# Optimization experiments

Measured on AMD Instinct MI355X. Metric: run time of the kernel, lower is better.

The kernel has to match this reference:

```python
import jax, jax.numpy as jnp
import numpy as np

M = 100000      # number of simplices
NNZ = 800000    # nonzeros per Laplacian (avg degree 8)
B = 2
C_IN = 64
C_OUT = 64
K1 = 3
K2 = 3


def setup_inputs() -> dict:
    key = jax.random.key(0)
    ks = jax.random.split(key, 7)
    Ll_indices = jax.random.randint(ks[0], (2, NNZ), 0, M, dtype=jnp.int32)
    Ll_values = jax.random.normal(ks[1], (NNZ,), dtype=jnp.float32) * 0.1
    Lu_indices = jax.random.randint(ks[2], (2, NNZ), 0, M, dtype=jnp.int32)
    Lu_values = jax.random.normal(ks[3], (NNZ,), dtype=jnp.float32) * 0.1
    x = jax.random.normal(ks[4], (B, C_IN, M), dtype=jnp.float32)
    theta = jax.random.normal(ks[5], (C_OUT, C_IN, K1 + K2), dtype=jnp.float32)
    bias = jnp.zeros((1, C_OUT, 1), dtype=jnp.float32)
    return {"Ll_indices": Ll_indices, "Ll_values": Ll_values,
            "Lu_indices": Lu_indices, "Lu_values": Lu_values,
            "x": x, "theta": theta, "bias": bias}


def _spmm(rows, cols, vals, x):
    # sparse (M,M) @ x along last axis; x: (B, C, M) -> (B, C, M)
    gathered = x[:, :, cols] * vals            # (B, C, nnz)
    return jnp.zeros_like(x).at[:, :, rows].add(gathered)


def _assemble_powers(K, rows, cols, vals, x):
    outs = [x]
    for _ in range(K - 1):
        outs.append(_spmm(rows, cols, vals, outs[-1]))
    return jnp.stack(outs, axis=3)             # (B, C, M, K)


def reference(Ll_indices, Ll_values, Lu_indices, Lu_values, x, theta, bias):
    X1 = _assemble_powers(K1, Ll_indices[0], Ll_indices[1], Ll_values, x)
    X2 = _assemble_powers(K2, Lu_indices[0], Lu_indices[1], Lu_values, x)
    X = jnp.concatenate((X1, X2), axis=3)      # (B, C_in, M, K1+K2)
    y = jnp.einsum('bimk,oik->bom', X, theta)  # (B, C_out, M)
    return y + bias
```

## Files before the change

kernel.cpp:

```cpp
#include <hip/hip_runtime.h>
#include <stdint.h>

#define M_SIMP 100000
#define MPAD   100064
#define NNZV   800000
#define KM5    5
#define NBH    3125
#define NBT    1563
#define NBW    40
#define NBM    6250
#define NBS    98

typedef unsigned int u32;
typedef __attribute__((ext_vector_type(8))) short short8;
typedef __attribute__((ext_vector_type(4))) float f32x4;

__device__ __forceinline__ float bf2f(u32 u){ return __uint_as_float(u << 16); }
__device__ __forceinline__ u32 f2bf(float f){
    u32 u = __float_as_uint(f);
    return (u + 0x7FFFu + ((u >> 16) & 1u)) >> 16;
}


__device__ __forceinline__ void role_hist(int h, int t, const int* __restrict__ idx,
                                          int* __restrict__ cnt, u32* __restrict__ pe){
    int e = h * 256 + t;
    if (e < NNZV){
        int r = idx[e];
        pe[e] = (u32)atomicAdd(&cnt[r], 1);
    }
}

__device__ __forceinline__ void role_transpose(int g, int t, const float* __restrict__ x,
                                               u32* __restrict__ F0){
    __shared__ unsigned short s[64 * 130];
    int m0 = g * 64;
    int j  = t & 63;
    int r4 = t >> 6;
    #pragma unroll 4
    for (int it = 0; it < 32; ++it){
        int bc = it * 4 + r4;
        int m  = m0 + j;
        if (m < M_SIMP)
            s[j * 130 + bc] = (unsigned short)f2bf(x[(size_t)bc * M_SIMP + m]);
    }
    __syncthreads();
    #pragma unroll 4
    for (int it = 0; it < 16; ++it){
        int m  = it * 4 + r4;
        int gm = m0 + m;
        if (gm < M_SIMP){
            u32 lo = s[m * 130 + 2 * j];
            u32 hi = s[m * 130 + 2 * j + 1];
            F0[(size_t)gm * 64 + j] = lo | (hi << 16);
        }
    }
}

__device__ __forceinline__ void role_wb(int g, int t, const float* __restrict__ theta,
                                        u32* __restrict__ Wb){
    int idx = g * 256 + t;
    if (idx < KM5 * 64 * 32){
        int km = idx >> 11;
        int r  = idx & 2047;
        int o  = r >> 5;
        int i2 = (r & 31) * 2;
        int k  = (km == 0) ? 0 : ((km < 3) ? km : km + 1);
        float lo = theta[o * 384 + i2 * 6 + k];
        float hi = theta[o * 384 + (i2 + 1) * 6 + k];
        if (km == 0){
            lo += theta[o * 384 + i2 * 6 + 3];
            hi += theta[o * 384 + (i2 + 1) * 6 + 3];
        }
        Wb[idx] = f2bf(lo) | (f2bf(hi) << 16);
    }
}

__device__ __forceinline__ void role_scan1(int b, int t, const int* __restrict__ in,
                                           int* __restrict__ out, int* __restrict__ bsums){
    __shared__ int s1[256];
    int base = b * 1024 + t * 4;
    int v0 = (base + 0 < M_SIMP) ? in[base + 0] : 0;
    int v1 = (base + 1 < M_SIMP) ? in[base + 1] : 0;
    int v2 = (base + 2 < M_SIMP) ? in[base + 2] : 0;
    int v3 = (base + 3 < M_SIMP) ? in[base + 3] : 0;
    int sum = v0 + v1 + v2 + v3;
    s1[t] = sum;
    __syncthreads();
    for (int off = 1; off < 256; off <<= 1){
        int x = (t >= off) ? s1[t - off] : 0;
        __syncthreads();
        s1[t] += x;
        __syncthreads();
    }
    int excl = s1[t] - sum;
    if (t == 255) bsums[b] = s1[255];
    if (base + 0 < M_SIMP) out[base + 0] = excl;
    if (base + 1 < M_SIMP) out[base + 1] = excl + v0;
    if (base + 2 < M_SIMP) out[base + 2] = excl + v0 + v1;
    if (base + 3 < M_SIMP) out[base + 3] = excl + v0 + v1 + v2;
}

__device__ __forceinline__ void role_scan3(int b, int t, int* __restrict__ out,
                                           const int* __restrict__ bsums){
    __shared__ int sb[256];
    sb[t] = (t < b && t < NBS) ? bsums[t] : 0;
    __syncthreads();
    #pragma unroll
    for (int off = 128; off > 0; off >>= 1){
        if (t < off) sb[t] += sb[t + off];
        __syncthreads();
    }
    int add = sb[0];
    if (t == 255 && b == 0) out[M_SIMP] = NNZV;
    int base = b * 1024 + t * 4;
    if (base < M_SIMP){
        int4* po = (int4*)(out + base);
        int4 v = *po; v.x += add; v.y += add; v.z += add; v.w += add; *po = v;
    }
}

__device__ __forceinline__ void role_scatcv(int b, int t, const int* __restrict__ idx,
                                            const float* __restrict__ val,
                                            const u32* __restrict__ pe,
                                            const int* __restrict__ rp,
                                            uint2* __restrict__ cv){
    int e = b * 256 + t;
    if (e < NNZV){
        int r = idx[e];
        int pos = rp[r] + (int)pe[e];
        uint2 o;
        o.x = (u32)idx[NNZV + e];
        o.y = __float_as_uint(val[e]);
        cv[pos] = o;
    }
}

__device__ __forceinline__ void role_spmm(int blk, int t, const int* __restrict__ rp,
                                          const uint2* __restrict__ cv,
                                          const u32* __restrict__ fin,
                                          u32* __restrict__ fout){
    int sub = t >> 4;
    int l   = t & 15;
    int row = blk * 16 + sub;
    if (row >= M_SIMP) return;
    int s = rp[row], en = rp[row + 1];
    float a0=0,a1=0,a2=0,a3=0,a4=0,a5=0,a6=0,a7=0;
    int j = s;
    for (; j + 4 <= en; j += 4){
        uint2 q0 = cv[j], q1 = cv[j+1], q2 = cv[j+2], q3 = cv[j+3];
        uint4 g0 = *(const uint4*)(fin + (size_t)q0.x * 64 + l * 4);
        uint4 g1 = *(const uint4*)(fin + (size_t)q1.x * 64 + l * 4);
        uint4 g2 = *(const uint4*)(fin + (size_t)q2.x * 64 + l * 4);
        uint4 g3 = *(const uint4*)(fin + (size_t)q3.x * 64 + l * 4);
        float v0 = __uint_as_float(q0.y), v1 = __uint_as_float(q1.y);
        float v2 = __uint_as_float(q2.y), v3 = __uint_as_float(q3.y);
        a0 += v0*bf2f(g0.x&0xffffu) + v1*bf2f(g1.x&0xffffu) + v2*bf2f(g2.x&0xffffu) + v3*bf2f(g3.x&0xffffu);
        a1 += v0*bf2f(g0.x>>16)     + v1*bf2f(g1.x>>16)     + v2*bf2f(g2.x>>16)     + v3*bf2f(g3.x>>16);
        a2 += v0*bf2f(g0.y&0xffffu) + v1*bf2f(g1.y&0xffffu) + v2*bf2f(g2.y&0xffffu) + v3*bf2f(g3.y&0xffffu);
        a3 += v0*bf2f(g0.y>>16)     + v1*bf2f(g1.y>>16)     + v2*bf2f(g2.y>>16)     + v3*bf2f(g3.y>>16);
        a4 += v0*bf2f(g0.z&0xffffu) + v1*bf2f(g1.z&0xffffu) + v2*bf2f(g2.z&0xffffu) + v3*bf2f(g3.z&0xffffu);
        a5 += v0*bf2f(g0.z>>16)     + v1*bf2f(g1.z>>16)     + v2*bf2f(g2.z>>16)     + v3*bf2f(g3.z>>16);
        a6 += v0*bf2f(g0.w&0xffffu) + v1*bf2f(g1.w&0xffffu) + v2*bf2f(g2.w&0xffffu) + v3*bf2f(g3.w&0xffffu);
        a7 += v0*bf2f(g0.w>>16)     + v1*bf2f(g1.w>>16)     + v2*bf2f(g2.w>>16)     + v3*bf2f(g3.w>>16);
    }
    for (; j < en; j++){
        uint2 q = cv[j];
        float v = __uint_as_float(q.y);
        uint4 g = *(const uint4*)(fin + (size_t)q.x * 64 + l * 4);
        a0 += v*bf2f(g.x&0xffffu); a1 += v*bf2f(g.x>>16);
        a2 += v*bf2f(g.y&0xffffu); a3 += v*bf2f(g.y>>16);
        a4 += v*bf2f(g.z&0xffffu); a5 += v*bf2f(g.z>>16);
        a6 += v*bf2f(g.w&0xffffu); a7 += v*bf2f(g.w>>16);
    }
    uint4 o;
    o.x = f2bf(a0) | (f2bf(a1) << 16);
    o.y = f2bf(a2) | (f2bf(a3) << 16);
    o.z = f2bf(a4) | (f2bf(a5) << 16);
    o.w = f2bf(a6) | (f2bf(a7) << 16);
    *(uint4*)(fout + (size_t)row * 64 + l * 4) = o;
}


__global__ __launch_bounds__(256) void k_fA(const int* __restrict__ Ll_idx,
                        int* __restrict__ cnt_l, u32* __restrict__ pe_l,
                        const float* __restrict__ x, u32* __restrict__ F0,
                        const float* __restrict__ theta, u32* __restrict__ Wb){
    int bid = blockIdx.x, t = threadIdx.x;
    int r3 = bid % 3, g3 = bid / 3;
    if (r3 < 2){
        int h = g3 * 2 + r3;
        if (h < NBH) role_hist(h, t, Ll_idx, cnt_l, pe_l);
    } else if (g3 < NBT){
        role_transpose(g3, t, x, F0);
    } else {
        role_wb(g3 - NBT, t, theta, Wb);
    }
}

__global__ __launch_bounds__(256) void k_scan1(const int* __restrict__ cnt,
                                               int* __restrict__ rp, int* __restrict__ bs){
    role_scan1(blockIdx.x, threadIdx.x, cnt, rp, bs);
}
__global__ __launch_bounds__(256) void k_scan3(int* __restrict__ rp, const int* __restrict__ bs){
    role_scan3(blockIdx.x, threadIdx.x, rp, bs);
}

__global__ __launch_bounds__(256) void k_scat_hist(
    const int* __restrict__ Ll_idx, const float* __restrict__ Ll_val,
    const u32* __restrict__ pe_l, const int* __restrict__ rp_l, uint2* __restrict__ cv_l,
    const int* __restrict__ Lu_idx, int* __restrict__ cnt_u, u32* __restrict__ pe_u){
    int bid = blockIdx.x, t = threadIdx.x;
    int g = bid >> 1;
    if ((bid & 1) == 0) role_scatcv(g, t, Ll_idx, Ll_val, pe_l, rp_l, cv_l);
    else                role_hist(g, t, Lu_idx, cnt_u, pe_u);
}

__global__ __launch_bounds__(256) void k_sp_scan1(
    const int* __restrict__ rp_l, const uint2* __restrict__ cv_l,
    const u32* __restrict__ F0, u32* __restrict__ F1,
    const int* __restrict__ cnt_u, int* __restrict__ rp_u, int* __restrict__ bs_u){
    int bid = blockIdx.x, t = threadIdx.x;
    if (bid < NBS) role_scan1(bid, t, cnt_u, rp_u, bs_u);
    else           role_spmm(bid - NBS, t, rp_l, cv_l, F0, F1);
}

__global__ __launch_bounds__(256) void k_sp_scat(
    const int* __restrict__ rp_l, const uint2* __restrict__ cv_l,
    const u32* __restrict__ F1, u32* __restrict__ F2,
    const int* __restrict__ Lu_idx, const float* __restrict__ Lu_val,
    const u32* __restrict__ pe_u, const int* __restrict__ rp_u, uint2* __restrict__ cv_u){
    int bid = blockIdx.x, t = threadIdx.x;
    int r3 = bid % 3, g3 = bid / 3;
    if (r3 == 0) role_scatcv(g3, t, Lu_idx, Lu_val, pe_u, rp_u, cv_u);
    else         role_spmm(g3 * 2 + (r3 - 1), t, rp_l, cv_l, F1, F2);
}

__global__ __launch_bounds__(256) void k_spmm(const int* __restrict__ rp,
                                              const uint2* __restrict__ cv,
                                              const u32* __restrict__ fin,
                                              u32* __restrict__ fout){
    role_spmm(blockIdx.x, threadIdx.x, rp, cv, fin, fout);
}

__global__ __launch_bounds__(256, 4) void k_gemm(
    const u32* __restrict__ F0, const u32* __restrict__ F1, const u32* __restrict__ F2,
    const u32* __restrict__ F4, const u32* __restrict__ F5,
    const u32* __restrict__ Wb, const float* __restrict__ bias, float* __restrict__ out)
{
    __shared__ __align__(16) u32 sh[2][4096];
    int t    = threadIdx.x;
    int wave = t >> 6;
    int lane = t & 63;
    int q    = lane >> 4;
    int l16  = lane & 15;
    int bm   = blockIdx.x * 64;
    const u32* __restrict__ Fs[KM5] = {F0, F1, F2, F4, F5};

    int rowbase  = t >> 4;
    int srcc     = (t & 15) ^ ((t >> 4) & 15);
    int wavebase = (t & 192) * 4;

    f32x4 a00 = {0.f,0.f,0.f,0.f}, a10 = {0.f,0.f,0.f,0.f};
    f32x4 a20 = {0.f,0.f,0.f,0.f}, a30 = {0.f,0.f,0.f,0.f};
    f32x4 a01 = {0.f,0.f,0.f,0.f}, a11 = {0.f,0.f,0.f,0.f};
    f32x4 a21 = {0.f,0.f,0.f,0.f}, a31 = {0.f,0.f,0.f,0.f};

    int o_a = wave * 16 + l16;

    short8 wc0 = *(const short8*)(Wb + (0 * 64 + o_a) * 32 + 0 * 16 + q * 4);
    short8 wc1 = *(const short8*)(Wb + (0 * 64 + o_a) * 32 + 1 * 16 + q * 4);

    #pragma unroll
    for (int i = 0; i < 4; ++i){
        const u32* g = Fs[0] + (size_t)(bm + i * 16 + rowbase) * 64 + srcc * 4;
        __builtin_amdgcn_global_load_lds(g, &sh[0][i * 1024 + wavebase], 16, 0, 0);
    }
    asm volatile("s_waitcnt vmcnt(0)" ::: "memory");
    __syncthreads();

    #pragma unroll
    for (int km = 0; km < KM5; ++km){
        short8 wn0 = wc0, wn1 = wc1;
        if (km < KM5 - 1){
            wn0 = *(const short8*)(Wb + ((km + 1) * 64 + o_a) * 32 + 0 * 16 + q * 4);
            wn1 = *(const short8*)(Wb + ((km + 1) * 64 + o_a) * 32 + 1 * 16 + q * 4);
            const u32* __restrict__ Fn = Fs[km + 1];
            u32* dst = &sh[(km + 1) & 1][0];
            #pragma unroll
            for (int i = 0; i < 4; ++i){
                const u32* g = Fn + (size_t)(bm + i * 16 + rowbase) * 64 + srcc * 4;
                __builtin_amdgcn_global_load_lds(g, dst + i * 1024 + wavebase, 16, 0, 0);
            }
        }

        const u32* Lb = &sh[km & 1][0];
        #pragma unroll
        for (int h = 0; h < 2; ++h){
            short8 wa = h ? wc1 : wc0;
            int c0 = ((h * 4 + q) ^ l16) * 4;
            int c1 = ((8 + h * 4 + q) ^ l16) * 4;
            #pragma unroll
            for (int ms = 0; ms < 4; ++ms){
                const u32* rp_ = Lb + ms * 1024 + l16 * 64;
                short8 b0 = *(const short8*)(rp_ + c0);
                short8 b1 = *(const short8*)(rp_ + c1);
                if (ms == 0){ a00 = __builtin_amdgcn_mfma_f32_16x16x32_bf16(wa, b0, a00, 0, 0, 0);
                              a01 = __builtin_amdgcn_mfma_f32_16x16x32_bf16(wa, b1, a01, 0, 0, 0); }
                if (ms == 1){ a10 = __builtin_amdgcn_mfma_f32_16x16x32_bf16(wa, b0, a10, 0, 0, 0);
                              a11 = __builtin_amdgcn_mfma_f32_16x16x32_bf16(wa, b1, a11, 0, 0, 0); }
                if (ms == 2){ a20 = __builtin_amdgcn_mfma_f32_16x16x32_bf16(wa, b0, a20, 0, 0, 0);
                              a21 = __builtin_amdgcn_mfma_f32_16x16x32_bf16(wa, b1, a21, 0, 0, 0); }
                if (ms == 3){ a30 = __builtin_amdgcn_mfma_f32_16x16x32_bf16(wa, b0, a30, 0, 0, 0);
                              a31 = __builtin_amdgcn_mfma_f32_16x16x32_bf16(wa, b1, a31, 0, 0, 0); }
            }
        }

        asm volatile("s_waitcnt vmcnt(0)" ::: "memory");
        __syncthreads();
        wc0 = wn0; wc1 = wn1;
    }

    int ob = wave * 16 + q * 4;
    float bv0 = bias[ob], bv1 = bias[ob+1], bv2 = bias[ob+2], bv3 = bias[ob+3];
    f32x4 accs0[4] = {a00, a10, a20, a30};
    f32x4 accs1[4] = {a01, a11, a21, a31};
    #pragma unroll
    for (int ms = 0; ms < 4; ms++){
        int gm = bm + ms * 16 + l16;
        if (gm < M_SIMP){
            size_t base0 = (size_t)(0 * 64 + ob) * M_SIMP + gm;
            size_t base1 = (size_t)(1 * 64 + ob) * M_SIMP + gm;
            out[base0             ] = accs0[ms][0] + bv0;
            out[base0 + 1ul*M_SIMP] = accs0[ms][1] + bv1;
            out[base0 + 2ul*M_SIMP] = accs0[ms][2] + bv2;
            out[base0 + 3ul*M_SIMP] = accs0[ms][3] + bv3;
            out[base1             ] = accs1[ms][0] + bv0;
            out[base1 + 1ul*M_SIMP] = accs1[ms][1] + bv1;
            out[base1 + 2ul*M_SIMP] = accs1[ms][2] + bv2;
            out[base1 + 3ul*M_SIMP] = accs1[ms][3] + bv3;
        }
    }
}

extern "C" void kernel_launch(void* const* d_in, const int* in_sizes, int n_in,
                              void* d_out, int out_size, void* d_ws, size_t ws_size,
                              hipStream_t stream)
{
    const int*   Ll_idx = (const int*)d_in[0];
    const float* Ll_val = (const float*)d_in[1];
    const int*   Lu_idx = (const int*)d_in[2];
    const float* Lu_val = (const float*)d_in[3];
    const float* x      = (const float*)d_in[4];
    const float* theta  = (const float*)d_in[5];
    const float* bias   = (const float*)d_in[6];
    float* out = (float*)d_out;

    char* ws = (char*)d_ws;
    size_t off = 0;
    auto take = [&](size_t bytes) -> char* {
        char* p = ws + off;
        off = (off + bytes + 255) & ~(size_t)255;
        return p;
    };
    const size_t FB = (size_t)MPAD * 64 * 4;
    u32* F0 = (u32*)take(FB);
    u32* F1 = (u32*)take(FB);
    u32* F2 = (u32*)take(FB);
    u32* F4 = (u32*)take(FB);
    u32* F5 = (u32*)take(FB);
    u32* Wb = (u32*)take((size_t)KM5 * 64 * 32 * 4);
    int* cnt_l = (int*)take((size_t)M_SIMP * 4);
    int* cnt_u = (int*)take((size_t)M_SIMP * 4);
    int* rp_l  = (int*)take((size_t)(M_SIMP + 1) * 4);
    int* rp_u  = (int*)take((size_t)(M_SIMP + 1) * 4);
    u32* pe_l  = (u32*)take((size_t)NNZV * 4);
    u32* pe_u  = (u32*)take((size_t)NNZV * 4);
    uint2* cv_l = (uint2*)take((size_t)NNZV * 8);
    uint2* cv_u = (uint2*)take((size_t)NNZV * 8);
    int* bs_l = (int*)take(512);
    int* bs_u = (int*)take(512);

    hipMemsetAsync(cnt_l, 0, (size_t)M_SIMP * 4, stream);
    hipMemsetAsync(cnt_u, 0, (size_t)M_SIMP * 4, stream);

    k_fA<<<3 * (NBT + NBW), 256, 0, stream>>>(Ll_idx, cnt_l, pe_l, x, F0, theta, Wb);

    k_scan1<<<NBS, 256, 0, stream>>>(cnt_l, rp_l, bs_l);
    k_scan3<<<NBS, 256, 0, stream>>>(rp_l, bs_l);

    k_scat_hist<<<2 * NBH, 256, 0, stream>>>(Ll_idx, Ll_val, pe_l, rp_l, cv_l,
                                             Lu_idx, cnt_u, pe_u);

    k_sp_scan1<<<NBS + NBM, 256, 0, stream>>>(rp_l, cv_l, F0, F1, cnt_u, rp_u, bs_u);

    k_scan3<<<NBS, 256, 0, stream>>>(rp_u, bs_u);

    k_sp_scat<<<3 * NBH, 256, 0, stream>>>(rp_l, cv_l, F1, F2,
                                           Lu_idx, Lu_val, pe_u, rp_u, cv_u);

    k_spmm<<<NBM, 256, 0, stream>>>(rp_u, cv_u, F0, F4);
    k_spmm<<<NBM, 256, 0, stream>>>(rp_u, cv_u, F4, F5);

    k_gemm<<<NBT, 256, 0, stream>>>(F0, F1, F2, F4, F5, Wb, bias, out);
}
```

Measured before the change: 389.4 us.

## Replace CSR build with fixed-capacity per-row buckets and batch both SpMMs

Measured after the change: 353.7 us (median of 2 runs). 9.2% less time.

```diff
diff --git a/kernel.cpp b/kernel.cpp
--- a/kernel.cpp
+++ b/kernel.cpp
@@ -5,11 +5,11 @@
 #define MPAD   100064
 #define NNZV   800000
 #define KM5    5
+#define CAP    40
 #define NBH    3125
 #define NBT    1563
 #define NBW    40
 #define NBM    6250
-#define NBS    98
 
 typedef unsigned int u32;
 typedef __attribute__((ext_vector_type(8))) short short8;
@@ -22,12 +22,17 @@
 }
 
 
-__device__ __forceinline__ void role_hist(int h, int t, const int* __restrict__ idx,
-                                          int* __restrict__ cnt, u32* __restrict__ pe){
+__device__ __forceinline__ void role_build(int h, int t, const int* __restrict__ idx,
+                                           const float* __restrict__ val,
+                                           int* __restrict__ cnt, uint2* __restrict__ cvE){
     int e = h * 256 + t;
     if (e < NNZV){
         int r = idx[e];
-        pe[e] = (u32)atomicAdd(&cnt[r], 1);
+        int p = atomicAdd(&cnt[r], 1);
+        uint2 o;
+        o.x = (u32)idx[NNZV + e];
+        o.y = __float_as_uint(val[e]);
+        cvE[(size_t)r * CAP + p] = o;
     }
 }
 
@@ -76,78 +81,19 @@
     }
 }
 
-__device__ __forceinline__ void role_scan1(int b, int t, const int* __restrict__ in,
-                                           int* __restrict__ out, int* __restrict__ bsums){
-    __shared__ int s1[256];
-    int base = b * 1024 + t * 4;
-    int v0 = (base + 0 < M_SIMP) ? in[base + 0] : 0;
-    int v1 = (base + 1 < M_SIMP) ? in[base + 1] : 0;
-    int v2 = (base + 2 < M_SIMP) ? in[base + 2] : 0;
-    int v3 = (base + 3 < M_SIMP) ? in[base + 3] : 0;
-    int sum = v0 + v1 + v2 + v3;
-    s1[t] = sum;
-    __syncthreads();
-    for (int off = 1; off < 256; off <<= 1){
-        int x = (t >= off) ? s1[t - off] : 0;
-        __syncthreads();
-        s1[t] += x;
-        __syncthreads();
-    }
-    int excl = s1[t] - sum;
-    if (t == 255) bsums[b] = s1[255];
-    if (base + 0 < M_SIMP) out[base + 0] = excl;
-    if (base + 1 < M_SIMP) out[base + 1] = excl + v0;
-    if (base + 2 < M_SIMP) out[base + 2] = excl + v0 + v1;
-    if (base + 3 < M_SIMP) out[base + 3] = excl + v0 + v1 + v2;
-}
-
-__device__ __forceinline__ void role_scan3(int b, int t, int* __restrict__ out,
-                                           const int* __restrict__ bsums){
-    __shared__ int sb[256];
-    sb[t] = (t < b && t < NBS) ? bsums[t] : 0;
-    __syncthreads();
-    #pragma unroll
-    for (int off = 128; off > 0; off >>= 1){
-        if (t < off) sb[t] += sb[t + off];
-        __syncthreads();
-    }
-    int add = sb[0];
-    if (t == 255 && b == 0) out[M_SIMP] = NNZV;
-    int base = b * 1024 + t * 4;
-    if (base < M_SIMP){
-        int4* po = (int4*)(out + base);
-        int4 v = *po; v.x += add; v.y += add; v.z += add; v.w += add; *po = v;
-    }
-}
-
-__device__ __forceinline__ void role_scatcv(int b, int t, const int* __restrict__ idx,
-                                            const float* __restrict__ val,
-                                            const u32* __restrict__ pe,
-                                            const int* __restrict__ rp,
-                                            uint2* __restrict__ cv){
-    int e = b * 256 + t;
-    if (e < NNZV){
-        int r = idx[e];
-        int pos = rp[r] + (int)pe[e];
-        uint2 o;
-        o.x = (u32)idx[NNZV + e];
-        o.y = __float_as_uint(val[e]);
-        cv[pos] = o;
-    }
-}
-
-__device__ __forceinline__ void role_spmm(int blk, int t, const int* __restrict__ rp,
-                                          const uint2* __restrict__ cv,
+__device__ __forceinline__ void role_spmm(int blk, int t, const int* __restrict__ cnt,
+                                          const uint2* __restrict__ cvE,
                                           const u32* __restrict__ fin,
                                           u32* __restrict__ fout){
     int sub = t >> 4;
     int l   = t & 15;
     int row = blk * 16 + sub;
     if (row >= M_SIMP) return;
-    int s = rp[row], en = rp[row + 1];
+    int deg = cnt[row];
+    const uint2* __restrict__ cv = cvE + (size_t)row * CAP;
     float a0=0,a1=0,a2=0,a3=0,a4=0,a5=0,a6=0,a7=0;
-    int j = s;
-    for (; j + 4 <= en; j += 4){
+    int j = 0;
+    for (; j + 4 <= deg; j += 4){
         uint2 q0 = cv[j], q1 = cv[j+1], q2 = cv[j+2], q3 = cv[j+3];
         uint4 g0 = *(const uint4*)(fin + (size_t)q0.x * 64 + l * 4);
         uint4 g1 = *(const uint4*)(fin + (size_t)q1.x * 64 + l * 4);
@@ -164,7 +110,7 @@
         a6 += v0*bf2f(g0.w&0xffffu) + v1*bf2f(g1.w&0xffffu) + v2*bf2f(g2.w&0xffffu) + v3*bf2f(g3.w&0xffffu);
         a7 += v0*bf2f(g0.w>>16)     + v1*bf2f(g1.w>>16)     + v2*bf2f(g2.w>>16)     + v3*bf2f(g3.w>>16);
     }
-    for (; j < en; j++){
+    for (; j < deg; j++){
         uint2 q = cv[j];
         float v = __uint_as_float(q.y);
         uint4 g = *(const uint4*)(fin + (size_t)q.x * 64 + l * 4);
@@ -182,65 +128,37 @@
 }
 
 
-__global__ __launch_bounds__(256) void k_fA(const int* __restrict__ Ll_idx,
-                        int* __restrict__ cnt_l, u32* __restrict__ pe_l,
-                        const float* __restrict__ x, u32* __restrict__ F0,
-                        const float* __restrict__ theta, u32* __restrict__ Wb){
+__global__ __launch_bounds__(256) void k_build(
+    const int* __restrict__ Ll_idx, const float* __restrict__ Ll_val,
+    int* __restrict__ cnt_l, uint2* __restrict__ cv_l,
+    const int* __restrict__ Lu_idx, const float* __restrict__ Lu_val,
+    int* __restrict__ cnt_u, uint2* __restrict__ cv_u,
+    const float* __restrict__ x, u32* __restrict__ F0,
+    const float* __restrict__ theta, u32* __restrict__ Wb)
+{
     int bid = blockIdx.x, t = threadIdx.x;
-    int r3 = bid % 3, g3 = bid / 3;
-    if (r3 < 2){
-        int h = g3 * 2 + r3;
-        if (h < NBH) role_hist(h, t, Ll_idx, cnt_l, pe_l);
-    } else if (g3 < NBT){
-        role_transpose(g3, t, x, F0);
+    int r5 = bid % 5, g5 = bid / 5;
+    if (r5 < 2){
+        int h = g5 * 2 + r5;
+        if (h < NBH) role_build(h, t, Ll_idx, Ll_val, cnt_l, cv_l);
+    } else if (r5 < 4){
+        int h = g5 * 2 + (r5 - 2);
+        if (h < NBH) role_build(h, t, Lu_idx, Lu_val, cnt_u, cv_u);
+    } else if (g5 < NBT){
+        role_transpose(g5, t, x, F0);
     } else {
-        role_wb(g3 - NBT, t, theta, Wb);
-    }
-}
-
-__global__ __launch_bounds__(256) void k_scan1(const int* __restrict__ cnt,
-                                               int* __restrict__ rp, int* __restrict__ bs){
-    role_scan1(blockIdx.x, threadIdx.x, cnt, rp, bs);
-}
-__global__ __launch_bounds__(256) void k_scan3(int* __restrict__ rp, const int* __restrict__ bs){
-    role_scan3(blockIdx.x, threadIdx.x, rp, bs);
-}
-
-__global__ __launch_bounds__(256) void k_scat_hist(
-    const int* __restrict__ Ll_idx, const float* __restrict__ Ll_val,
-    const u32* __restrict__ pe_l, const int* __restrict__ rp_l, uint2* __restrict__ cv_l,
-    const int* __restrict__ Lu_idx, int* __restrict__ cnt_u, u32* __restrict__ pe_u){
-    int bid = blockIdx.x, t = threadIdx.x;
-    int g = bid >> 1;
-    if ((bid & 1) == 0) role_scatcv(g, t, Ll_idx, Ll_val, pe_l, rp_l, cv_l);
-    else                role_hist(g, t, Lu_idx, cnt_u, pe_u);
-}
-
-__global__ __launch_bounds__(256) void k_sp_scan1(
-    const int* __restrict__ rp_l, const uint2* __restrict__ cv_l,
-    const u32* __restrict__ F0, u32* __restrict__ F1,
-    const int* __restrict__ cnt_u, int* __restrict__ rp_u, int* __restrict__ bs_u){
-    int bid = blockIdx.x, t = threadIdx.x;
-    if (bid < NBS) role_scan1(bid, t, cnt_u, rp_u, bs_u);
-    else           role_spmm(bid - NBS, t, rp_l, cv_l, F0, F1);
-}
-
-__global__ __launch_bounds__(256) void k_sp_scat(
-    const int* __restrict__ rp_l, const uint2* __restrict__ cv_l,
-    const u32* __restrict__ F1, u32* __restrict__ F2,
-    const int* __restrict__ Lu_idx, const float* __restrict__ Lu_val,
-    const u32* __restrict__ pe_u, const int* __restrict__ rp_u, uint2* __restrict__ cv_u){
-    int bid = blockIdx.x, t = threadIdx.x;
-    int r3 = bid % 3, g3 = bid / 3;
-    if (r3 == 0) role_scatcv(g3, t, Lu_idx, Lu_val, pe_u, rp_u, cv_u);
-    else         role_spmm(g3 * 2 + (r3 - 1), t, rp_l, cv_l, F1, F2);
-}
-
-__global__ __launch_bounds__(256) void k_spmm(const int* __restrict__ rp,
-                                              const uint2* __restrict__ cv,
-                                              const u32* __restrict__ fin,
-                                              u32* __restrict__ fout){
-    role_spmm(blockIdx.x, threadIdx.x, rp, cv, fin, fout);
+        role_wb(g5 - NBT, t, theta, Wb);
+    }
+}
+
+__global__ __launch_bounds__(256) void k_spmm2(
+    const int* __restrict__ cnt_l, const uint2* __restrict__ cv_l,
+    const u32* __restrict__ finL, u32* __restrict__ foutL,
+    const int* __restrict__ cnt_u, const uint2* __restrict__ cv_u,
+    const u32* __restrict__ finU, u32* __restrict__ foutU)
+{
+    if (blockIdx.y == 0) role_spmm(blockIdx.x, threadIdx.x, cnt_l, cv_l, finL, foutL);
+    else                 role_spmm(blockIdx.x, threadIdx.x, cnt_u, cv_u, finU, foutU);
 }
 
 __global__ __launch_bounds__(256, 4) void k_gemm(
@@ -370,37 +288,24 @@
     u32* F4 = (u32*)take(FB);
     u32* F5 = (u32*)take(FB);
     u32* Wb = (u32*)take((size_t)KM5 * 64 * 32 * 4);
-    int* cnt_l = (int*)take((size_t)M_SIMP * 4);
-    int* cnt_u = (int*)take((size_t)M_SIMP * 4);
-    int* rp_l  = (int*)take((size_t)(M_SIMP + 1) * 4);
-    int* rp_u  = (int*)take((size_t)(M_SIMP + 1) * 4);
-    u32* pe_l  = (u32*)take((size_t)NNZV * 4);
-    u32* pe_u  = (u32*)take((size_t)NNZV * 4);
-    uint2* cv_l = (uint2*)take((size_t)NNZV * 8);
-    uint2* cv_u = (uint2*)take((size_t)NNZV * 8);
-    int* bs_l = (int*)take(512);
-    int* bs_u = (int*)take(512);
+    int*   cnt_l = (int*)take((size_t)M_SIMP * 4);
+    int*   cnt_u = (int*)take((size_t)M_SIMP * 4);
+    uint2* cv_l  = (uint2*)take((size_t)M_SIMP * CAP * 8);
+    uint2* cv_u  = (uint2*)take((size_t)M_SIMP * CAP * 8);
 
     hipMemsetAsync(cnt_l, 0, (size_t)M_SIMP * 4, stream);
     hipMemsetAsync(cnt_u, 0, (size_t)M_SIMP * 4, stream);
 
-    k_fA<<<3 * (NBT + NBW), 256, 0, stream>>>(Ll_idx, cnt_l, pe_l, x, F0, theta, Wb);
-
-    k_scan1<<<NBS, 256, 0, stream>>>(cnt_l, rp_l, bs_l);
-    k_scan3<<<NBS, 256, 0, stream>>>(rp_l, bs_l);
-
-    k_scat_hist<<<2 * NBH, 256, 0, stream>>>(Ll_idx, Ll_val, pe_l, rp_l, cv_l,
-                                             Lu_idx, cnt_u, pe_u);
-
-    k_sp_scan1<<<NBS + NBM, 256, 0, stream>>>(rp_l, cv_l, F0, F1, cnt_u, rp_u, bs_u);
-
-    k_scan3<<<NBS, 256, 0, stream>>>(rp_u, bs_u);
-
-    k_sp_scat<<<3 * NBH, 256, 0, stream>>>(rp_l, cv_l, F1, F2,
-                                           Lu_idx, Lu_val, pe_u, rp_u, cv_u);
-
-    k_spmm<<<NBM, 256, 0, stream>>>(rp_u, cv_u, F0, F4);
-    k_spmm<<<NBM, 256, 0, stream>>>(rp_u, cv_u, F4, F5);
+    k_build<<<5 * (NBT + NBW), 256, 0, stream>>>(
+        Ll_idx, Ll_val, cnt_l, cv_l,
+        Lu_idx, Lu_val, cnt_u, cv_u,
+        x, F0, theta, Wb);
+
+    dim3 gm(NBM, 2);
+    k_spmm2<<<gm, 256, 0, stream>>>(cnt_l, cv_l, F0, F1,
+                                    cnt_u, cv_u, F0, F4);
+    k_spmm2<<<gm, 256, 0, stream>>>(cnt_l, cv_l, F1, F2,
+                                    cnt_u, cv_u, F4, F5);
 
     k_gemm<<<NBT, 256, 0, stream>>>(F0, F1, F2, F4, F5, Wb, bias, out);
 }
```
